# Optimization experiments

Measured on AMD Instinct MI355X. Metric: run time of the kernel, lower is better.

## Reference

```python
import jax, jax.numpy as jnp
import numpy as np

FP8_MAX = 448.0  # torch.finfo(torch.float8_e4m3fn).max
FP8_MIN = -448.0


def per_tensor_quantize(t):
    # amax = max(|min|, |max|) over the whole tensor
    amax = jnp.maximum(jnp.abs(jnp.min(t)), jnp.abs(jnp.max(t)))
    scale = FP8_MAX / jnp.clip(amax, 1e-12, None)
    q = jnp.clip(t * scale, FP8_MIN, FP8_MAX).astype(jnp.float8_e4m3fn)
    inv_scale = (1.0 / scale).astype(jnp.float32)
    return q, inv_scale


def setup_inputs() -> dict:
    key = jax.random.key(0)
    k1, k2 = jax.random.split(key)
    B, S, D_IN, D_OUT = 8, 8192, 1024, 1024
    x = jax.random.normal(k1, (B, S, D_IN), dtype=jnp.float32)
    w = jax.random.normal(k2, (D_OUT, D_IN), dtype=jnp.float32) * 0.02
    qweight, weight_scale = per_tensor_quantize(w)  # fp8 weight + scalar fp32 scale
    return {"x": x, "qweight": qweight, "weight_scale": weight_scale}


def reference(x, qweight, weight_scale):
    # dynamic per-tensor activation quantization (quantize -> fp8)
    qinput, act_scale = per_tensor_quantize(x)
    # fp8 gemm with inline dequant scales (manual dequant-linear path, bias=None)
    A = qinput.astype(x.dtype) * act_scale          # [B, S, D_in]
    W = qweight.astype(x.dtype) * weight_scale.astype(x.dtype)  # [D_out, D_in]
    out = jnp.einsum('bsk,nk->bsn', A, W)           # [B, S, D_out]
    return out
```

## Files before the change

### kernel.cpp

```cpp
#include <hip/hip_runtime.h>
#include <hip/hip_fp8.h>
#include <stdint.h>
#include <cmath>

using f32x4 = __attribute__((ext_vector_type(4))) float;
using i32x4 = __attribute__((ext_vector_type(4))) int;
using i32x8 = __attribute__((ext_vector_type(8))) int;

#define FP8MAX 448.0f

__device__ __forceinline__ void gload_lds16(const void* g, void* l) {
  __builtin_amdgcn_global_load_lds(
      (const __attribute__((address_space(1))) unsigned int*)g,
      (__attribute__((address_space(3))) unsigned int*)l,
      16, 0, 0);
}

__device__ __forceinline__ uint8_t to_fp8(float v) {
  __hip_fp8_e4m3 q(fminf(fmaxf(v, -FP8MAX), FP8MAX));
  return q.__x;
}

__global__ void wdetect(const uint8_t* __restrict__ w, unsigned int* __restrict__ flag) {
  const float* wf = (const float*)w;
  const unsigned short* wh = (const unsigned short*)w;
  int f32ok = 1, bf16ok = 1;
  for (int i = threadIdx.x; i < 4096; i += 256) {
    float v = wf[i];
    if (!(isfinite(v) && fabsf(v) <= FP8MAX)) f32ok = 0;
    else { __hip_fp8_e4m3 q(v); if ((float)q != v) f32ok = 0; }
    float hv = __uint_as_float(((unsigned int)wh[i]) << 16);
    if (!(isfinite(hv) && fabsf(hv) <= FP8MAX)) bf16ok = 0;
    else { __hip_fp8_e4m3 qh(hv); if ((float)qh != hv) bf16ok = 0; }
  }
  __shared__ int sf, sb;
  if (threadIdx.x == 0) { sf = 1; sb = 1; }
  __syncthreads();
  if (!f32ok) atomicAnd(&sf, 0);
  if (!bf16ok) atomicAnd(&sb, 0);
  __syncthreads();
  if (threadIdx.x == 0) *flag = sf ? 2u : (sb ? 1u : 0u);
}

__global__ void wconv(const uint8_t* __restrict__ w, uint8_t* __restrict__ q,
                      const unsigned int* __restrict__ flag_p, int n) {
  unsigned int f = *flag_p;
  int i0 = (blockIdx.x * blockDim.x + threadIdx.x) * 4;
  if (i0 >= n) return;
  uint32_t out;
  if (f == 2) {
    float4 v = *(const float4*)((const float*)w + i0);
    out = (uint32_t)to_fp8(v.x) | ((uint32_t)to_fp8(v.y) << 8) |
          ((uint32_t)to_fp8(v.z) << 16) | ((uint32_t)to_fp8(v.w) << 24);
  } else if (f == 1) {
    ushort4 h = *(const ushort4*)((const unsigned short*)w + i0);
    float a = __uint_as_float(((unsigned int)h.x) << 16);
    float b = __uint_as_float(((unsigned int)h.y) << 16);
    float c = __uint_as_float(((unsigned int)h.z) << 16);
    float d = __uint_as_float(((unsigned int)h.w) << 16);
    out = (uint32_t)to_fp8(a) | ((uint32_t)to_fp8(b) << 8) |
          ((uint32_t)to_fp8(c) << 16) | ((uint32_t)to_fp8(d) << 24);
  } else {
    out = *(const uint32_t*)(w + i0);
  }
  *(uint32_t*)(q + i0) = out;
}

__global__ void amax_kernel(const float* __restrict__ x, size_t n4,
                            unsigned int* __restrict__ amax_u) {
  const float4* x4 = (const float4*)x;
  float m = 0.0f;
  size_t stride = (size_t)gridDim.x * blockDim.x;
  for (size_t i = (size_t)blockIdx.x * blockDim.x + threadIdx.x; i < n4; i += stride) {
    float4 v = x4[i];
    m = fmaxf(m, fmaxf(fmaxf(fabsf(v.x), fabsf(v.y)),
                       fmaxf(fabsf(v.z), fabsf(v.w))));
  }
  #pragma unroll
  for (int off = 32; off > 0; off >>= 1)
    m = fmaxf(m, __shfl_xor(m, off));
  __shared__ float sm[16];
  int wid = threadIdx.x >> 6;
  if ((threadIdx.x & 63) == 0) sm[wid] = m;
  __syncthreads();
  if (threadIdx.x == 0) {
    int nw = blockDim.x >> 6;
    float r = sm[0];
    for (int i = 1; i < nw; i++) r = fmaxf(r, sm[i]);
    atomicMax(amax_u, __float_as_uint(r));
  }
}

__global__ void quant_kernel(const float* __restrict__ x,
                             uint8_t* __restrict__ q,
                             const float* __restrict__ amax_p, size_t n16) {
  float amax = fmaxf(amax_p[0], 1e-12f);
  float scale = FP8MAX / amax;
  const float4* x4 = (const float4*)x;
  uint4* q16 = (uint4*)q;
  size_t stride = (size_t)gridDim.x * blockDim.x;
  for (size_t i = (size_t)blockIdx.x * blockDim.x + threadIdx.x; i < n16; i += stride) {
    uint32_t w[4];
    #pragma unroll
    for (int j = 0; j < 4; j++) {
      float4 v = x4[i * 4 + j];
      w[j] = (uint32_t)to_fp8(v.x * scale) | ((uint32_t)to_fp8(v.y * scale) << 8) |
             ((uint32_t)to_fp8(v.z * scale) << 16) | ((uint32_t)to_fp8(v.w * scale) << 24);
    }
    uint4 o; o.x = w[0]; o.y = w[1]; o.z = w[2]; o.w = w[3];
    q16[i] = o;
  }
}

#define BM 128
#define BN 128
#define BK 128

__global__ __launch_bounds__(256) void gemm_fp8(
    const uint8_t* __restrict__ A,
    const uint8_t* __restrict__ B,
    float* __restrict__ C,
    const float* __restrict__ amax_p,
    const float* __restrict__ wscale_p,
    int M, int N, int K) {
  __shared__ uint8_t lds_a[BM * BK];
  __shared__ uint8_t lds_b[BN * BK];

  int nwg = gridDim.x;
  int cpx = nwg >> 3;
  int swz = (blockIdx.x & 7) * cpx + (blockIdx.x >> 3);

  int nstrips = N / BN;
  int bm = (swz / nstrips) * BM;
  int bn = (swz % nstrips) * BN;

  int t = threadIdx.x;
  int lane = t & 63;
  int wave = t >> 6;
  int wm = (wave >> 1) * 64;
  int wn = (wave & 1) * 64;

  float amax = fmaxf(amax_p[0], 1e-12f);
  float scale = FP8MAX / amax;
  float s = (1.0f / scale) * wscale_p[0];

  f32x4 acc[4][4] = {};

  const int rt = t >> 3;
  const int ct = t & 7;
  uint8_t* la = &lds_a[wave * 1024];
  uint8_t* lb = &lds_b[wave * 1024];

  const int lr = lane & 15;
  const int x7 = lr & 7;
  const int g2 = (lane >> 4) << 1;
  const int c0 = ((g2 ^ x7) << 4);
  const int c1 = (((g2 + 1) ^ x7) << 4);
  int abase[4], bbase[4];
  #pragma unroll
  for (int i = 0; i < 4; i++) abase[i] = (wm + i * 16 + lr) * BK;
  #pragma unroll
  for (int j = 0; j < 4; j++) bbase[j] = (wn + j * 16 + lr) * BK;

  for (int k0 = 0; k0 < K; k0 += BK) {
    __syncthreads();
    #pragma unroll
    for (int p = 0; p < 4; ++p) {
      int r = p * 32 + rt;
      int gc = (ct ^ (r & 7)) * 16;
      gload_lds16(A + (size_t)(bm + r) * K + k0 + gc, la + p * 4096);
      gload_lds16(B + (size_t)(bn + r) * K + k0 + gc, lb + p * 4096);
    }
    __syncthreads();

    i32x8 af[4], bf[4];
    #pragma unroll
    for (int i = 0; i < 4; i++) {
      i32x4 lo = *(const i32x4*)&lds_a[abase[i] + c0];
      i32x4 hi = *(const i32x4*)&lds_a[abase[i] + c1];
      af[i] = (i32x8){lo.x, lo.y, lo.z, lo.w, hi.x, hi.y, hi.z, hi.w};
    }
    #pragma unroll
    for (int j = 0; j < 4; j++) {
      i32x4 lo = *(const i32x4*)&lds_b[bbase[j] + c0];
      i32x4 hi = *(const i32x4*)&lds_b[bbase[j] + c1];
      bf[j] = (i32x8){lo.x, lo.y, lo.z, lo.w, hi.x, hi.y, hi.z, hi.w};
    }
    #pragma unroll
    for (int i = 0; i < 4; i++)
      #pragma unroll
      for (int j = 0; j < 4; j++)
        acc[i][j] = __builtin_amdgcn_mfma_scale_f32_16x16x128_f8f6f4(
            af[i], bf[j], acc[i][j],
            0 , 0 ,
            0, 0x7f7f7f7f,
            0, 0x7f7f7f7f);
  }

  #pragma unroll
  for (int i = 0; i < 4; i++) {
    #pragma unroll
    for (int j = 0; j < 4; j++) {
      int row = bm + wm + i * 16 + (lane >> 4) * 4;
      int col = bn + wn + j * 16 + (lane & 15);
      #pragma unroll
      for (int r = 0; r < 4; r++)
        C[(size_t)(row + r) * N + col] = acc[i][j][r] * s;
    }
  }
}

extern "C" void kernel_launch(void* const* d_in, const int* in_sizes, int n_in,
                              void* d_out, int out_size, void* d_ws, size_t ws_size,
                              hipStream_t stream) {
  const float* x = (const float*)d_in[0];
  const uint8_t* wraw = (const uint8_t*)d_in[1];
  const float* wscale = (const float*)d_in[2];
  float* out = (float*)d_out;

  long long in0 = in_sizes[0];
  long long in1 = in_sizes[1];
  double kd = sqrt((double)in0 * (double)in1 / (double)out_size);
  long long K = (long long)(kd + 0.5);
  long long M = in0 / K;
  long long N = in1 / K;

  unsigned int* amax_u = (unsigned int*)d_ws;
  const float* amax_f = (const float*)d_ws;
  unsigned int* wflag = (unsigned int*)((uint8_t*)d_ws + 64);
  uint8_t* qw = (uint8_t*)d_ws + 4096;
  uint8_t* qx = (uint8_t*)d_ws + (2u << 20);

  hipMemsetAsync(d_ws, 0, 4, stream);
  wdetect<<<1, 256, 0, stream>>>(wraw, wflag);
  wconv<<<(unsigned)(in1 / 4 / 256), 256, 0, stream>>>(wraw, qw, wflag, (int)in1);
  amax_kernel<<<2048, 256, 0, stream>>>(x, (size_t)(in0 / 4), amax_u);
  quant_kernel<<<2048, 256, 0, stream>>>(x, qx, amax_f, (size_t)(in0 / 16));

  dim3 grid((unsigned)((M / BM) * (N / BN)));
  gemm_fp8<<<grid, 256, 0, stream>>>(qx, qw, out, amax_f, wscale,
                                     (int)M, (int)N, (int)K);
}
```

Measured before the change: 277.6 us.

## Double-buffer LDS in fp8 GEMM and fold weight detection into conversion kernel

The GEMM main loop now uses two LDS buffers, so the global-to-LDS load of the next K tile is issued while MFMAs run on the current one, with one barrier per tile instead of two. The separate weight-detection kernel and the memset are merged into wconv: every block repeats the detection scan and block 0 zeroes the amax word, which removes two launches. LDS use doubles to 64KB per workgroup, which may reduce occupancy. The K loop steps by two tiles, so it assumes an even tile count.

Result: slower. 283.2 us (+2.0%).

```diff
diff --git a/kernel.cpp b/kernel.cpp
--- a/kernel.cpp
+++ b/kernel.cpp
@@ -21,14 +21,17 @@
   return q.__x;
 }
 
-__global__ void wdetect(const uint8_t* __restrict__ w, unsigned int* __restrict__ flag) {
+__global__ void wconv(const uint8_t* __restrict__ w, uint8_t* __restrict__ q,
+                      unsigned int* __restrict__ amax_u, int n) {
+  if (blockIdx.x == 0 && threadIdx.x == 0) amax_u[0] = 0u;
+
   const float* wf = (const float*)w;
   const unsigned short* wh = (const unsigned short*)w;
   int f32ok = 1, bf16ok = 1;
   for (int i = threadIdx.x; i < 4096; i += 256) {
     float v = wf[i];
     if (!(isfinite(v) && fabsf(v) <= FP8MAX)) f32ok = 0;
-    else { __hip_fp8_e4m3 q(v); if ((float)q != v) f32ok = 0; }
+    else { __hip_fp8_e4m3 qq(v); if ((float)qq != v) f32ok = 0; }
     float hv = __uint_as_float(((unsigned int)wh[i]) << 16);
     if (!(isfinite(hv) && fabsf(hv) <= FP8MAX)) bf16ok = 0;
     else { __hip_fp8_e4m3 qh(hv); if ((float)qh != hv) bf16ok = 0; }
@@ -39,12 +42,8 @@
   if (!f32ok) atomicAnd(&sf, 0);
   if (!bf16ok) atomicAnd(&sb, 0);
   __syncthreads();
-  if (threadIdx.x == 0) *flag = sf ? 2u : (sb ? 1u : 0u);
-}
-
-__global__ void wconv(const uint8_t* __restrict__ w, uint8_t* __restrict__ q,
-                      const unsigned int* __restrict__ flag_p, int n) {
-  unsigned int f = *flag_p;
+  unsigned int f = sf ? 2u : (sb ? 1u : 0u);
+
   int i0 = (blockIdx.x * blockDim.x + threadIdx.x) * 4;
   if (i0 >= n) return;
   uint32_t out;
@@ -123,8 +122,8 @@
     const float* __restrict__ amax_p,
     const float* __restrict__ wscale_p,
     int M, int N, int K) {
-  __shared__ uint8_t lds_a[BM * BK];
-  __shared__ uint8_t lds_b[BN * BK];
+  __shared__ uint8_t lds_a[2][BM * BK];
+  __shared__ uint8_t lds_b[2][BN * BK];
 
   int nwg = gridDim.x;
   int cpx = nwg >> 3;
@@ -148,8 +147,7 @@
 
   const int rt = t >> 3;
   const int ct = t & 7;
-  uint8_t* la = &lds_a[wave * 1024];
-  uint8_t* lb = &lds_b[wave * 1024];
+  const int stoff = wave * 1024;
 
   const int lr = lane & 15;
   const int x7 = lr & 7;
@@ -162,28 +160,28 @@
   #pragma unroll
   for (int j = 0; j < 4; j++) bbase[j] = (wn + j * 16 + lr) * BK;
 
-  for (int k0 = 0; k0 < K; k0 += BK) {
-    __syncthreads();
+  auto stage = [&](uint8_t* dstA, uint8_t* dstB, int k0) {
     #pragma unroll
     for (int p = 0; p < 4; ++p) {
       int r = p * 32 + rt;
       int gc = (ct ^ (r & 7)) * 16;
-      gload_lds16(A + (size_t)(bm + r) * K + k0 + gc, la + p * 4096);
-      gload_lds16(B + (size_t)(bn + r) * K + k0 + gc, lb + p * 4096);
-    }
-    __syncthreads();
-
+      gload_lds16(A + (size_t)(bm + r) * K + k0 + gc, dstA + stoff + p * 4096);
+      gload_lds16(B + (size_t)(bn + r) * K + k0 + gc, dstB + stoff + p * 4096);
+    }
+  };
+
+  auto compute = [&](const uint8_t* baseA, const uint8_t* baseB) {
     i32x8 af[4], bf[4];
     #pragma unroll
     for (int i = 0; i < 4; i++) {
-      i32x4 lo = *(const i32x4*)&lds_a[abase[i] + c0];
-      i32x4 hi = *(const i32x4*)&lds_a[abase[i] + c1];
+      i32x4 lo = *(const i32x4*)(baseA + abase[i] + c0);
+      i32x4 hi = *(const i32x4*)(baseA + abase[i] + c1);
       af[i] = (i32x8){lo.x, lo.y, lo.z, lo.w, hi.x, hi.y, hi.z, hi.w};
     }
     #pragma unroll
     for (int j = 0; j < 4; j++) {
-      i32x4 lo = *(const i32x4*)&lds_b[bbase[j] + c0];
-      i32x4 hi = *(const i32x4*)&lds_b[bbase[j] + c1];
+      i32x4 lo = *(const i32x4*)(baseB + bbase[j] + c0);
+      i32x4 hi = *(const i32x4*)(baseB + bbase[j] + c1);
       bf[j] = (i32x8){lo.x, lo.y, lo.z, lo.w, hi.x, hi.y, hi.z, hi.w};
     }
     #pragma unroll
@@ -195,6 +193,19 @@
             0 , 0 ,
             0, 0x7f7f7f7f,
             0, 0x7f7f7f7f);
+  };
+
+  const int KITERS = K / BK;
+  stage(lds_a[0], lds_b[0], 0);
+  __syncthreads();
+
+  for (int it = 0; it < KITERS; it += 2) {
+    if (it + 1 < KITERS) stage(lds_a[1], lds_b[1], (it + 1) * BK);
+    compute(lds_a[0], lds_b[0]);
+    __syncthreads();
+    if (it + 2 < KITERS) stage(lds_a[0], lds_b[0], (it + 2) * BK);
+    compute(lds_a[1], lds_b[1]);
+    __syncthreads();
   }
 
   #pragma unroll
@@ -227,13 +238,10 @@
 
   unsigned int* amax_u = (unsigned int*)d_ws;
   const float* amax_f = (const float*)d_ws;
-  unsigned int* wflag = (unsigned int*)((uint8_t*)d_ws + 64);
   uint8_t* qw = (uint8_t*)d_ws + 4096;
   uint8_t* qx = (uint8_t*)d_ws + (2u << 20);
 
-  hipMemsetAsync(d_ws, 0, 4, stream);
-  wdetect<<<1, 256, 0, stream>>>(wraw, wflag);
-  wconv<<<(unsigned)(in1 / 4 / 256), 256, 0, stream>>>(wraw, qw, wflag, (int)in1);
+  wconv<<<(unsigned)(in1 / 4 / 256), 256, 0, stream>>>(wraw, qw, amax_u, (int)in1);
   amax_kernel<<<2048, 256, 0, stream>>>(x, (size_t)(in0 / 4), amax_u);
   quant_kernel<<<2048, 256, 0, stream>>>(x, qx, amax_f, (size_t)(in0 / 16));
 
```
